# Optimization experiments

Measured on AMD Instinct MI355X. Metric: run time of the kernel, lower is better.

## Reference

```python
import jax, jax.numpy as jnp
import numpy as np
from jax import lax

B, C_IN, C_OUT, K, H, W, NUM = 32, 256, 256, 3, 28, 28, 8


def setup_inputs() -> dict:
    key = jax.random.key(0)
    k1, k2, k3 = jax.random.split(key, 3)
    inputs = jax.random.normal(k1, (B, C_IN, H, W), dtype=jnp.float32)
    inputs_se = jax.random.uniform(k2, (B, NUM), dtype=jnp.float32)
    # weight bank [out*in*k*k, num], init scale sqrt(1/(c*k*k)) as in the module
    scale = np.sqrt(1.0 / (C_IN * K * K)).astype(np.float32)
    weight = jax.random.normal(k3, (C_OUT * C_IN * K * K, NUM), dtype=jnp.float32) * scale
    bias = jnp.zeros((C_OUT,), dtype=jnp.float32)
    return {"inputs": inputs, "inputs_se": inputs_se, "weight": weight, "bias": bias}


def reference(inputs, inputs_se, weight, bias):
    b, c, h, w = inputs.shape
    out_ch = bias.shape[0]
    # per-sample filter generation: [B, num] @ [num, out*in*k*k] -> [B, out, in, k, k]
    wgen = jnp.einsum('bn,on->bo', inputs_se, weight).reshape(b, out_ch, c, K, K)

    def conv_one(x, wk):
        # x: [C,H,W], wk: [O,C,K,K] -> [O,H,W]  (stride 1, padding 1)
        return lax.conv_general_dilated(
            x[None], wk,
            window_strides=(1, 1), padding=[(1, 1), (1, 1)],
            dimension_numbers=('NCHW', 'OIHW', 'NCHW'))[0]

    out = jax.vmap(conv_one)(inputs, wgen)  # [B, O, H, W]
    return out + bias[None, :, None, None]
```

## Files before the change

### kernel.cpp

```cpp
#include <hip/hip_runtime.h>
#include <hip/hip_fp16.h>

#define BB    32
#define CIN   256
#define COUT  256
#define HH    28
#define WW    28
#define NPIX  784
#define KD    2304
#define HP    30
#define WP    30

#define BM    128
#define BN    128
#define NT    7

#define WGEN_ELEMS ((size_t)BB * COUT * KD)
#define XPAD_OFF   (WGEN_ELEMS)

typedef _Float16 f16x8 __attribute__((ext_vector_type(8)));
typedef float    f32x4 __attribute__((ext_vector_type(4)));

static __device__ __forceinline__ ushort f2h_bits(float v) {
    __half h = __float2half(v);
    return *reinterpret_cast<ushort*>(&h);
}

static __device__ __forceinline__ void gll16(const ushort* g, ushort* l) {
    __builtin_amdgcn_global_load_lds(
        (const __attribute__((address_space(1))) unsigned int*)g,
        (__attribute__((address_space(3))) unsigned int*)l, 16, 0, 0);
}

__global__ __launch_bounds__(256) void gen_w(const float* __restrict__ weight,
                                             const float* __restrict__ se,
                                             ushort* __restrict__ wgen) {
    const int o = blockIdx.x;
    const int c = threadIdx.x;

    __shared__ float  se_sh[BB * 8];
    __shared__ ushort w_sh[KD];

    se_sh[c] = se[c];

    float4 wr[18];
    const float4* wp = (const float4*)(weight + (size_t)(o * CIN + c) * 9 * 8);
#pragma unroll
    for (int i = 0; i < 18; ++i) wr[i] = wp[i];
    __syncthreads();

    for (int b = 0; b < BB; ++b) {
        const float s0 = se_sh[b * 8 + 0], s1 = se_sh[b * 8 + 1];
        const float s2 = se_sh[b * 8 + 2], s3 = se_sh[b * 8 + 3];
        const float s4 = se_sh[b * 8 + 4], s5 = se_sh[b * 8 + 5];
        const float s6 = se_sh[b * 8 + 6], s7 = se_sh[b * 8 + 7];
#pragma unroll
        for (int khw = 0; khw < 9; ++khw) {
            const float4 w0 = wr[khw * 2 + 0];
            const float4 w1 = wr[khw * 2 + 1];
            const float v = w0.x * s0 + w0.y * s1 + w0.z * s2 + w0.w * s3
                          + w1.x * s4 + w1.y * s5 + w1.z * s6 + w1.w * s7;
            w_sh[khw * 256 + c] = f2h_bits(v);
        }
        __syncthreads();
        const uint4* src = (const uint4*)w_sh;
        uint4* dst = (uint4*)(wgen + ((size_t)b * COUT + o) * KD);
        dst[c] = src[c];
        if (c < 32) dst[256 + c] = src[256 + c];
        __syncthreads();
    }
}

__global__ __launch_bounds__(256) void gen_x(const float* __restrict__ x,
                                             ushort* __restrict__ xpad) {
    const int bid = blockIdx.x;
    const int hp  = bid % HP;
    const int b   = bid / HP;
    const int tid = threadIdx.x;

    ushort* row = xpad + ((size_t)b * HP + hp) * WP * CIN;

    if (hp == 0 || hp == HP - 1) {
        uint* r32 = (uint*)row;
        for (int i = tid; i < (WP * CIN) / 2; i += 256) r32[i] = 0u;
        return;
    }
    {
        uint* c0 = (uint*)row;
        uint* c1 = (uint*)(row + (WP - 1) * CIN);
        if (tid < 128)       c0[tid] = 0u;
        else                 c1[tid - 128] = 0u;
    }

    __shared__ float lds[CIN * (WW + 1)];
    const int h = hp - 1;
    const float* xr = x + (size_t)b * CIN * NPIX + h * WW;

    for (int f = tid; f < CIN * WW; f += 256) {
        const int c = f / WW;
        const int w = f % WW;
        lds[c * (WW + 1) + w] = xr[(size_t)c * NPIX + w];
    }
    __syncthreads();
    for (int g = tid; g < WW * CIN; g += 256) {
        const int w = g >> 8;
        const int c = g & 255;
        row[(w + 1) * CIN + c] = f2h_bits(lds[c * (WW + 1) + w]);
    }
}

__global__ __launch_bounds__(256) void dconv_mfma(const ushort* __restrict__ wgen,
                                                  const ushort* __restrict__ xpad,
                                                  const float* __restrict__ bias,
                                                  float* __restrict__ out) {
    const int bid   = blockIdx.x;
    const int g     = bid & 7;
    const int s     = bid >> 3;
    const int nt    = s % NT;
    const int slice = g + 8 * (s / NT);
    const int b     = slice >> 1;
    const int mt    = slice & 1;

    const int tid  = threadIdx.x;
    const int lane = tid & 63;
    const int wave = tid >> 6;
    const int wm   = wave >> 1;
    const int wn   = wave & 1;
    const int col  = lane & 15;
    const int quad = lane >> 4;

    __shared__ ushort Ash[BM * 32];
    __shared__ ushort Psh[4 * 8 * 30 * 8];

    const int mo   = mt * BM + wm * 64;
    const int no   = nt * BN + wn * 64;
    const int h_lo = (nt * BN) / WW;

    int  pixbase[4];
    int  pst[4];
#pragma unroll
    for (int j = 0; j < 4; ++j) {
        const int p  = no + j * 16 + col;
        pst[j] = p;
        const int pc = p > (NPIX - 1) ? (NPIX - 1) : p;
        const int h  = pc / WW;
        const int w  = pc % WW;
        pixbase[j] = (h - h_lo) * 30 + w;
    }

    const int s_sw  = (col >> 1) & 3;
    const int abase = ((wm * 64 + col) << 2) + (quad ^ s_sw);

    const ushort* wg = wgen + ((size_t)b * COUT + mt * BM) * KD;
    const ushort* xp = xpad + (size_t)b * HP * WP * CIN;

    f32x4 acc[4][4];
#pragma unroll
    for (int mi = 0; mi < 4; ++mi)
#pragma unroll
        for (int nj = 0; nj < 4; ++nj)
            acc[mi][nj] = (f32x4){0.f, 0.f, 0.f, 0.f};

    for (int c32 = 0; c32 < 8; ++c32) {
        __syncthreads();

#pragma unroll
        for (int r = 0; r < 4; ++r) {
            const int j = r * 256 + tid;
            if (j < 960) {
                const int qc  = j / 240;
                const int rem = j % 240;
                const int rr  = rem / 30;
                const int ww  = rem % 30;
                int srow = h_lo + rr;
                if (srow > 29) srow = 29;
                gll16(xp + ((size_t)srow * WP + ww) * CIN + c32 * 32 + qc * 8,
                      Psh + (size_t)j * 8);
            }
        }
#pragma unroll
        for (int r = 0; r < 2; ++r) {
            const int cch = r * 256 + tid;
            const int m   = cch >> 2;
            const int kc  = (cch & 3) ^ ((m >> 1) & 3);
            gll16(wg + ((size_t)m * 9 + 0) * CIN + c32 * 32 + kc * 8,
                  Ash + (size_t)cch * 8);
        }

#pragma unroll
        for (int khw = 0; khw < 9; ++khw) {
            if (khw > 0) {
                __syncthreads();
#pragma unroll
                for (int r = 0; r < 2; ++r) {
                    const int cch = r * 256 + tid;
                    const int m   = cch >> 2;
                    const int kc  = (cch & 3) ^ ((m >> 1) & 3);
                    gll16(wg + ((size_t)m * 9 + khw) * CIN + c32 * 32 + kc * 8,
                          Ash + (size_t)cch * 8);
                }
            }
            __syncthreads();

            const int koff = (khw / 3) * 30 + (khw % 3);

            f16x8 af[4];
#pragma unroll
            for (int sub = 0; sub < 4; ++sub)
                af[sub] = ((const f16x8*)Ash)[abase + sub * 64];

            f16x8 bf[4];
#pragma unroll
            for (int j = 0; j < 4; ++j)
                bf[j] = ((const f16x8*)Psh)[quad * 240 + pixbase[j] + koff];

#pragma unroll
            for (int mi = 0; mi < 4; ++mi)
#pragma unroll
                for (int nj = 0; nj < 4; ++nj)
                    acc[mi][nj] = __builtin_amdgcn_mfma_f32_16x16x32_f16(
                        af[mi], bf[nj], acc[mi][nj], 0, 0, 0);
        }
    }

    float* ob = out + (size_t)b * COUT * NPIX;
#pragma unroll
    for (int mi = 0; mi < 4; ++mi) {
        const int m = mo + mi * 16 + quad * 4;
        const float4 bv = *(const float4*)(bias + m);
#pragma unroll
        for (int nj = 0; nj < 4; ++nj) {
            const int p = pst[nj];
            if (p < NPIX) {
                ob[(size_t)(m + 0) * NPIX + p] = acc[mi][nj][0] + bv.x;
                ob[(size_t)(m + 1) * NPIX + p] = acc[mi][nj][1] + bv.y;
                ob[(size_t)(m + 2) * NPIX + p] = acc[mi][nj][2] + bv.z;
                ob[(size_t)(m + 3) * NPIX + p] = acc[mi][nj][3] + bv.w;
            }
        }
    }
}

extern "C" void kernel_launch(void* const* d_in, const int* in_sizes, int n_in,
                              void* d_out, int out_size, void* d_ws, size_t ws_size,
                              hipStream_t stream) {
    const float* x      = (const float*)d_in[0];
    const float* se     = (const float*)d_in[1];
    const float* weight = (const float*)d_in[2];
    const float* bias   = (const float*)d_in[3];
    float* out          = (float*)d_out;

    ushort* wgen = (ushort*)d_ws;
    ushort* xpad = (ushort*)d_ws + XPAD_OFF;
    (void)ws_size; (void)in_sizes; (void)n_in; (void)out_size;

    gen_w<<<dim3(COUT), dim3(256), 0, stream>>>(weight, se, wgen);
    gen_x<<<dim3(BB * HP), dim3(256), 0, stream>>>(x, xpad);
    dconv_mfma<<<dim3(BB * 2 * NT), dim3(256), 0, stream>>>(wgen, xpad, bias, out);
}
```

Before: 162.8 us.

## Double-buffer LDS tiles in dconv and split gen_w across batch groups

The conv kernel now double-buffers the weight and input-patch tiles in LDS and flattens the channel-chunk and tap loops into one 72-step loop. The load for the next step is issued before the current step's MFMAs, so global-to-LDS traffic can overlap compute, with one barrier per step instead of two. Global/LDS offsets are precomputed outside the loop. Separately, gen_w launches 8x more blocks, each handling 4 batches, to fill the GPU. The cost is double the LDS use in dconv, which may lower occupancy, and each gen_w block re-reads the weight bank.

```diff
diff --git a/kernel.cpp b/kernel.cpp
--- a/kernel.cpp
+++ b/kernel.cpp
@@ -35,8 +35,9 @@
 __global__ __launch_bounds__(256) void gen_w(const float* __restrict__ weight,
                                              const float* __restrict__ se,
                                              ushort* __restrict__ wgen) {
-    const int o = blockIdx.x;
-    const int c = threadIdx.x;
+    const int o  = blockIdx.x & 255;
+    const int bg = blockIdx.x >> 8;
+    const int c  = threadIdx.x;
 
     __shared__ float  se_sh[BB * 8];
     __shared__ ushort w_sh[KD];
@@ -49,7 +50,9 @@
     for (int i = 0; i < 18; ++i) wr[i] = wp[i];
     __syncthreads();
 
-    for (int b = 0; b < BB; ++b) {
+#pragma unroll
+    for (int bi = 0; bi < 4; ++bi) {
+        const int b = bg * 4 + bi;
         const float s0 = se_sh[b * 8 + 0], s1 = se_sh[b * 8 + 1];
         const float s2 = se_sh[b * 8 + 2], s3 = se_sh[b * 8 + 3];
         const float s4 = se_sh[b * 8 + 4], s5 = se_sh[b * 8 + 5];
@@ -129,31 +132,53 @@
     const int col  = lane & 15;
     const int quad = lane >> 4;
 
-    __shared__ ushort Ash[BM * 32];
-    __shared__ ushort Psh[4 * 8 * 30 * 8];
+    __shared__ ushort Ash[2][BM * 32];
+    __shared__ ushort Psh[2][4 * 8 * 30 * 8];
 
     const int mo   = mt * BM + wm * 64;
     const int no   = nt * BN + wn * 64;
     const int h_lo = (nt * BN) / WW;
 
-    int  pixbase[4];
-    int  pst[4];
+    const ushort* wg = wgen + ((size_t)b * COUT + mt * BM) * KD;
+    const ushort* xp = xpad + (size_t)b * HP * WP * CIN;
+
+    int a_goff[2], a_loff[2];
+#pragma unroll
+    for (int r = 0; r < 2; ++r) {
+        const int cch = r * 256 + tid;
+        const int m   = cch >> 2;
+        const int kc  = (cch & 3) ^ ((m >> 1) & 3);
+        a_goff[r] = m * 9 * CIN + kc * 8;
+        a_loff[r] = cch * 8;
+    }
+    int p_goff[4], p_loff[4];
+    bool p_ok[4];
+#pragma unroll
+    for (int r = 0; r < 4; ++r) {
+        const int j = r * 256 + tid;
+        p_ok[r] = (j < 960);
+        const int jj  = p_ok[r] ? j : 0;
+        const int qc  = jj / 240;
+        const int rem = jj % 240;
+        const int rr  = rem / 30;
+        const int ww  = rem % 30;
+        int srow = h_lo + rr;
+        if (srow > 29) srow = 29;
+        p_goff[r] = (srow * WP + ww) * CIN + qc * 8;
+        p_loff[r] = jj * 8;
+    }
+
+    int pixbase[4], pst[4];
 #pragma unroll
     for (int j = 0; j < 4; ++j) {
         const int p  = no + j * 16 + col;
         pst[j] = p;
         const int pc = p > (NPIX - 1) ? (NPIX - 1) : p;
-        const int h  = pc / WW;
-        const int w  = pc % WW;
-        pixbase[j] = (h - h_lo) * 30 + w;
-    }
-
+        pixbase[j] = (pc / WW - h_lo) * 30 + (pc % WW);
+    }
     const int s_sw  = (col >> 1) & 3;
     const int abase = ((wm * 64 + col) << 2) + (quad ^ s_sw);
 
-    const ushort* wg = wgen + ((size_t)b * COUT + mt * BM) * KD;
-    const ushort* xp = xpad + (size_t)b * HP * WP * CIN;
-
     f32x4 acc[4][4];
 #pragma unroll
     for (int mi = 0; mi < 4; ++mi)
@@ -161,66 +186,55 @@
         for (int nj = 0; nj < 4; ++nj)
             acc[mi][nj] = (f32x4){0.f, 0.f, 0.f, 0.f};
 
-    for (int c32 = 0; c32 < 8; ++c32) {
+#pragma unroll
+    for (int r = 0; r < 2; ++r)
+        gll16(wg + a_goff[r], &Ash[0][a_loff[r]]);
+#pragma unroll
+    for (int r = 0; r < 4; ++r)
+        if (p_ok[r]) gll16(xp + p_goff[r], &Psh[0][p_loff[r]]);
+
+    for (int step = 0; step < 72; ++step) {
+        const int khw  = step % 9;
+        const int c32  = step / 9;
+        const int abuf = step & 1;
+        const int pbuf = c32 & 1;
+
         __syncthreads();
 
-#pragma unroll
-        for (int r = 0; r < 4; ++r) {
-            const int j = r * 256 + tid;
-            if (j < 960) {
-                const int qc  = j / 240;
-                const int rem = j % 240;
-                const int rr  = rem / 30;
-                const int ww  = rem % 30;
-                int srow = h_lo + rr;
-                if (srow > 29) srow = 29;
-                gll16(xp + ((size_t)srow * WP + ww) * CIN + c32 * 32 + qc * 8,
-                      Psh + (size_t)j * 8);
+        if (step + 1 < 72) {
+            const int nkhw = (step + 1) % 9;
+            const int nc32 = (step + 1) / 9;
+            const int aoff = nkhw * 256 + nc32 * 32;
+#pragma unroll
+            for (int r = 0; r < 2; ++r)
+                gll16(wg + a_goff[r] + aoff, &Ash[abuf ^ 1][a_loff[r]]);
+            if (nkhw == 0) {
+                const int poff = nc32 * 32;
+#pragma unroll
+                for (int r = 0; r < 4; ++r)
+                    if (p_ok[r]) gll16(xp + p_goff[r] + poff,
+                                       &Psh[pbuf ^ 1][p_loff[r]]);
             }
         }
-#pragma unroll
-        for (int r = 0; r < 2; ++r) {
-            const int cch = r * 256 + tid;
-            const int m   = cch >> 2;
-            const int kc  = (cch & 3) ^ ((m >> 1) & 3);
-            gll16(wg + ((size_t)m * 9 + 0) * CIN + c32 * 32 + kc * 8,
-                  Ash + (size_t)cch * 8);
-        }
-
-#pragma unroll
-        for (int khw = 0; khw < 9; ++khw) {
-            if (khw > 0) {
-                __syncthreads();
-#pragma unroll
-                for (int r = 0; r < 2; ++r) {
-                    const int cch = r * 256 + tid;
-                    const int m   = cch >> 2;
-                    const int kc  = (cch & 3) ^ ((m >> 1) & 3);
-                    gll16(wg + ((size_t)m * 9 + khw) * CIN + c32 * 32 + kc * 8,
-                          Ash + (size_t)cch * 8);
-                }
-            }
-            __syncthreads();
-
-            const int koff = (khw / 3) * 30 + (khw % 3);
-
-            f16x8 af[4];
-#pragma unroll
-            for (int sub = 0; sub < 4; ++sub)
-                af[sub] = ((const f16x8*)Ash)[abase + sub * 64];
-
-            f16x8 bf[4];
-#pragma unroll
-            for (int j = 0; j < 4; ++j)
-                bf[j] = ((const f16x8*)Psh)[quad * 240 + pixbase[j] + koff];
-
-#pragma unroll
-            for (int mi = 0; mi < 4; ++mi)
-#pragma unroll
-                for (int nj = 0; nj < 4; ++nj)
-                    acc[mi][nj] = __builtin_amdgcn_mfma_f32_16x16x32_f16(
-                        af[mi], bf[nj], acc[mi][nj], 0, 0, 0);
-        }
+
+        const int koff = (khw / 3) * 30 + (khw % 3);
+
+        f16x8 af[4];
+#pragma unroll
+        for (int sub = 0; sub < 4; ++sub)
+            af[sub] = ((const f16x8*)Ash[abuf])[abase + sub * 64];
+
+        f16x8 bf[4];
+#pragma unroll
+        for (int j = 0; j < 4; ++j)
+            bf[j] = ((const f16x8*)Psh[pbuf])[quad * 240 + pixbase[j] + koff];
+
+#pragma unroll
+        for (int mi = 0; mi < 4; ++mi)
+#pragma unroll
+            for (int nj = 0; nj < 4; ++nj)
+                acc[mi][nj] = __builtin_amdgcn_mfma_f32_16x16x32_f16(
+                    af[mi], bf[nj], acc[mi][nj], 0, 0, 0);
     }
 
     float* ob = out + (size_t)b * COUT * NPIX;
@@ -254,7 +268,7 @@
     ushort* xpad = (ushort*)d_ws + XPAD_OFF;
     (void)ws_size; (void)in_sizes; (void)n_in; (void)out_size;
 
-    gen_w<<<dim3(COUT), dim3(256), 0, stream>>>(weight, se, wgen);
+    gen_w<<<dim3(COUT * 8), dim3(256), 0, stream>>>(weight, se, wgen);
     gen_x<<<dim3(BB * HP), dim3(256), 0, stream>>>(x, xpad);
     dconv_mfma<<<dim3(BB * 2 * NT), dim3(256), 0, stream>>>(wgen, xpad, bias, out);
 }
```

New measurement: 162.7 us. No clear change (-0.0%).
